# Kernel tuning notes

Hardware: AMD Instinct MI355X
Metric: run time of the kernel (lower is better)

Reference implementation:

```python
import jax, jax.numpy as jnp
import numpy as np

MU, SIGMA = -9.1232, 3.5412
FFT_SIZES = [8, 16, 32, 64]
HOP_SIZES = [2, 4, 8, 16]
EPS_MAG, EPS_SC = 1e-7, 1e-8


def hann_periodic(n):
    # torch.hann_window default (periodic=True)
    return 0.5 * (1.0 - jnp.cos(2.0 * jnp.pi * jnp.arange(n, dtype=jnp.float32) / n))


def stft_mag(xf, n_fft, hop):
    # xf: (rows, T). Matches torch.stft(center=True, pad_mode='reflect', onesided).
    pad = n_fft // 2
    xp = jnp.pad(xf, ((0, 0), (pad, pad)), mode='reflect')
    n_frames = 1 + (xp.shape[-1] - n_fft) // hop
    idx = jnp.arange(n_frames)[:, None] * hop + jnp.arange(n_fft)[None, :]
    frames = xp[:, idx] * hann_periodic(n_fft)  # (rows, n_frames, n_fft)
    spec = jnp.fft.rfft(frames, axis=-1)        # (rows, n_frames, n_fft//2+1)
    return jnp.abs(spec) + EPS_MAG


def setup_inputs() -> dict:
    key = jax.random.key(0)
    k1, k2 = jax.random.split(key)
    x = jax.random.normal(k1, (32, 1, 128, 1024), dtype=jnp.float32)
    y = jax.random.normal(k2, (32, 1, 128, 1024), dtype=jnp.float32)
    return {"x": x, "y": y}


def reference(x, y):
    B, C, F_mel, T = x.shape
    x_flat = jnp.exp(x * SIGMA + MU).reshape(-1, T)  # un-normalize log-mel -> linear
    y_flat = jnp.exp(y * SIGMA + MU).reshape(-1, T)
    loss_sc = jnp.float32(0.0)
    loss_mag = jnp.float32(0.0)
    for n_fft, hop in zip(FFT_SIZES, HOP_SIZES):
        x_mag = stft_mag(x_flat, n_fft, hop)
        y_mag = stft_mag(y_flat, n_fft, hop)
        sc = jnp.linalg.norm((y_mag - x_mag).ravel()) / (
            jnp.linalg.norm(y_mag.ravel()) + EPS_SC)
        mag = jnp.mean(jnp.abs(jnp.log(x_mag) - jnp.log(y_mag)))
        loss_sc = loss_sc + sc
        loss_mag = loss_mag + mag
    n = len(FFT_SIZES)
    return (loss_sc / n, loss_mag / n)
```

## Files before the change

### kernel.cpp

```cpp
#include <hip/hip_runtime.h>
#include <math.h>

static constexpr float kSigma = 3.5412f;
static constexpr float kMu    = -9.1232f;

constexpr double kPId = 3.14159265358979323846264338327950288;

constexpr double tp_sin(double r) {
    const double r2 = r * r;
    double t = r, s = r;
    t *= -r2 / (2.0 * 3.0);   s += t;
    t *= -r2 / (4.0 * 5.0);   s += t;
    t *= -r2 / (6.0 * 7.0);   s += t;
    t *= -r2 / (8.0 * 9.0);   s += t;
    t *= -r2 / (10.0 * 11.0); s += t;
    t *= -r2 / (12.0 * 13.0); s += t;
    return s;
}
constexpr double tp_cos(double r) {
    const double r2 = r * r;
    double t = 1.0, c = 1.0;
    t *= -r2 / (1.0 * 2.0);   c += t;
    t *= -r2 / (3.0 * 4.0);   c += t;
    t *= -r2 / (5.0 * 6.0);   c += t;
    t *= -r2 / (7.0 * 8.0);   c += t;
    t *= -r2 / (9.0 * 10.0);  c += t;
    t *= -r2 / (11.0 * 12.0); c += t;
    return c;
}
constexpr float ctw_c(int k, int n) {
    const int kk = ((k % n) + n) % n;
    const int q = (4 * kk) / n;
    const int num = 4 * kk - q * n;
    const double r = (2.0 * kPId * num) / (4.0 * n);
    const double cr = tp_cos(r), sr = tp_sin(r);
    return (float)(q == 0 ? cr : q == 1 ? -sr : q == 2 ? -cr : sr);
}
constexpr float ctw_ns(int k, int n) {
    const int kk = ((k % n) + n) % n;
    const int q = (4 * kk) / n;
    const int num = 4 * kk - q * n;
    const double r = (2.0 * kPId * num) / (4.0 * n);
    const double cr = tp_cos(r), sr = tp_sin(r);
    const double s = (q == 0 ? sr : q == 1 ? cr : q == 2 ? -sr : -cr);
    return (float)(-s);
}

#define DECLZ \
    float zxr0=0.f,zxi0=0.f,zyr0=0.f,zyi0=0.f,  zxr1=0.f,zxi1=0.f,zyr1=0.f,zyi1=0.f, \
          zxr2=0.f,zxi2=0.f,zyr2=0.f,zyi2=0.f,  zxr3=0.f,zxi3=0.f,zyr3=0.f,zyi3=0.f, \
          zxr4=0.f,zxi4=0.f,zyr4=0.f,zyi4=0.f,  zxr5=0.f,zxi5=0.f,zyr5=0.f,zyi5=0.f, \
          zxr6=0.f,zxi6=0.f,zyr6=0.f,zyi6=0.f,  zxr7=0.f,zxi7=0.f,zyr7=0.f,zyi7=0.f, \
          zxr8=0.f,zxi8=0.f,zyr8=0.f,zyi8=0.f,  zxr9=0.f,zxi9=0.f,zyr9=0.f,zyi9=0.f, \
          zxr10=0.f,zxi10=0.f,zyr10=0.f,zyi10=0.f, zxr11=0.f,zxi11=0.f,zyr11=0.f,zyi11=0.f; \
    (void)zxr0;(void)zxi0;(void)zyr0;(void)zyi0;(void)zxr11;(void)zxi11;(void)zyr11;(void)zyi11;

#define UPDB(n, m) \
    if constexpr ((n) >= 1 && (n) <= NB) { \
        constexpr int   k_ = (BSTART + (n) - 1) * ((m) + TAU * HH); \
        constexpr float c_ = ctw_c(k_, NN); \
        constexpr float s_ = ctw_ns(k_, NN); \
        zxr##n = fmaf(dx, c_, zxr##n);  zxi##n = fmaf(dx, s_, zxi##n); \
        zyr##n = fmaf(dy, c_, zyr##n);  zyi##n = fmaf(dy, s_, zyi##n); \
    }

#define ALLB(m) UPDB(1,m) UPDB(2,m) UPDB(3,m) UPDB(4,m) UPDB(5,m) \
                UPDB(6,m) UPDB(7,m) UPDB(8,m) UPDB(9,m) UPDB(10,m)

#define UPD_M(m) \
    if constexpr ((m) < HH) { \
        const float dx = px[off + TAU*HH + NN + (m)] - px[off + TAU*HH + (m)]; \
        const float dy = py[off + TAU*HH + NN + (m)] - py[off + TAU*HH + (m)]; \
        ALLB(m) \
    }
#define WRM_M(m) \
    if constexpr ((m) < HH) { \
        const float dx = px[TAU*HH + (m)]; \
        const float dy = py[TAU*HH + (m)]; \
        ALLB(m) \
    }

#define FORM(M) M(0) M(1) M(2) M(3) M(4) M(5) M(6) M(7) \
                M(8) M(9) M(10) M(11) M(12) M(13) M(14) M(15)

#define EMTB(nm, nc, np) \
    if constexpr (((nc) - 1) >= EJ0 && ((nc) - 1) < EJ0 + EN) { \
        constexpr int BG = BSTART + (nc) - 1; \
        float wxr, wxi, wyr, wyi; \
        if constexpr (BG == 0) { \
            const float sx_ = (PH==0) ? zxr##np : (PH==1) ? -zxi##np : (PH==2) ? -zxr##np : zxi##np; \
            const float sy_ = (PH==0) ? zyr##np : (PH==1) ? -zyi##np : (PH==2) ? -zyr##np : zyi##np; \
            wxr = 0.5f*zxr##nc - 0.5f*sx_;  wxi = 0.5f*zxi##nc; \
            wyr = 0.5f*zyr##nc - 0.5f*sy_;  wyi = 0.5f*zyi##nc; \
        } else if constexpr (BG == NN/2) { \
            const float sx_ = (PH==0) ? zxr##nm : (PH==1) ? zxi##nm : (PH==2) ? -zxr##nm : -zxi##nm; \
            const float sy_ = (PH==0) ? zyr##nm : (PH==1) ? zyi##nm : (PH==2) ? -zyr##nm : -zyi##nm; \
            wxr = 0.5f*zxr##nc - 0.5f*sx_;  wxi = 0.5f*zxi##nc; \
            wyr = 0.5f*zyr##nc - 0.5f*sy_;  wyi = 0.5f*zyi##nc; \
        } else { \
            const float txr = (PH==0) ? (zxr##nm + zxr##np) : (PH==1) ? (zxi##nm - zxi##np) \
                            : (PH==2) ? (-zxr##nm - zxr##np) : (zxi##np - zxi##nm); \
            const float txi = (PH==0) ? (zxi##nm + zxi##np) : (PH==1) ? (zxr##np - zxr##nm) \
                            : (PH==2) ? (-zxi##nm - zxi##np) : (zxr##nm - zxr##np); \
            const float tyr = (PH==0) ? (zyr##nm + zyr##np) : (PH==1) ? (zyi##nm - zyi##np) \
                            : (PH==2) ? (-zyr##nm - zyr##np) : (zyi##np - zyi##nm); \
            const float tyi = (PH==0) ? (zyi##nm + zyi##np) : (PH==1) ? (zyr##np - zyr##nm) \
                            : (PH==2) ? (-zyi##nm - zyi##np) : (zyr##nm - zyr##np); \
            wxr = fmaf(-0.25f, txr, 0.5f*zxr##nc);  wxi = fmaf(-0.25f, txi, 0.5f*zxi##nc); \
            wyr = fmaf(-0.25f, tyr, 0.5f*zyr##nc);  wyi = fmaf(-0.25f, tyi, 0.5f*zyi##nc); \
        } \
        const float pxm = fmaf(wxr, wxr, wxi*wxi); \
        const float pym = fmaf(wyr, wyr, wyi*wyi); \
        const float sm_ = pxm + pym; \
        const float rt_ = sqrtf(pxm * pym); \
        sd2 += fmaf(-2.0f, rt_, sm_); \
        sy2 += pym; \
        slg = fmaf(0.5f, fabsf(__logf(__fdividef(pxm + 1e-14f, pym + 1e-14f))), slg); \
    }

#define FOREMT(M) M(0,1,2) M(1,2,3) M(2,3,4) M(3,4,5) M(4,5,6) \
                  M(5,6,7) M(6,7,8) M(7,8,9) M(8,9,10) M(9,10,11)

#define SLOT(t) { constexpr int TAU = (t); constexpr int PH = (t); FOREMT(EMTB) FORM(UPD_M) }
#define WARM(t) { constexpr int TAU = (t); FORM(WRM_M) }

template <int NN, int BSTART, int NB, int EJ0, int EN, int OFF>
__device__ __forceinline__ void run_group(const float* __restrict__ px_,
                                          const float* __restrict__ py_,
                                          int seg, float& sd2, float& sy2, float& slg)
{
    constexpr int HH = NN / 4;
    constexpr int FF = 4096 / NN + 1;
    const int t0 = (seg * FF) >> 3;
    const int t1 = ((seg + 1) * FF) >> 3;
    const int L  = t1 - t0;
    const float* __restrict__ px = px_ + OFF + t0 * HH;
    const float* __restrict__ py = py_ + OFF + t0 * HH;

    DECLZ
    WARM(0) WARM(1) WARM(2) WARM(3)

    int off = 0;
    const int nq = L >> 2, rem = L & 3;
#pragma unroll 1
    for (int q = 0; q < nq; ++q) {
        SLOT(0) SLOT(1) SLOT(2) SLOT(3)
        off += 4 * HH;
    }
    if (rem > 0) { SLOT(0) }
    if (rem > 1) { SLOT(1) }
    if (rem > 2) { SLOT(2) }
}

__global__ __launch_bounds__(1024, 4)
void fused_sdft_kernel(const float* __restrict__ xg, const float* __restrict__ yg,
                       float* __restrict__ acc)
{
    constexpr int RS = 1106;
    __shared__ float ldsx[16][RS];
    __shared__ float ldsy[16][RS];
    __shared__ float red[16][3];

    const int tid  = threadIdx.x;
    const int row0 = blockIdx.x << 4;

#pragma unroll 1
    for (int task = tid; task < 8192; task += 1024) {
        const int q = task & 255, rr = (task >> 8) & 15, sig = task >> 12;
        const float* __restrict__ src = sig ? yg : xg;
        const float4 v = reinterpret_cast<const float4*>(src)[((row0 + rr) << 8) + q];
        float* dst = sig ? &ldsy[rr][32 + (q << 2)] : &ldsx[rr][32 + (q << 2)];
        dst[0] = __expf(fmaf(v.x, kSigma, kMu));
        dst[1] = __expf(fmaf(v.y, kSigma, kMu));
        dst[2] = __expf(fmaf(v.z, kSigma, kMu));
        dst[3] = __expf(fmaf(v.w, kSigma, kMu));
    }
#pragma unroll 1
    for (int task = tid; task < 2560; task += 1024) {
        const int p = task % 80, rem_ = task / 80;
        const int rr = rem_ & 15, sig = rem_ >> 4;
        const int j = (p < 32) ? p : (1024 + p);
        float v = 0.f;
        if (j < 1088) {
            const int i = (j < 32) ? (32 - j) : (2078 - j);
            const float* __restrict__ src = sig ? yg : xg;
            v = __expf(fmaf(src[((row0 + rr) << 10) + i], kSigma, kMu));
        }
        (sig ? ldsy[rr] : ldsx[rr])[j] = v;
    }
    __syncthreads();

    const int wid = tid >> 6, lane = tid & 63;
    const int seg = ((wid & 1) << 2) + (lane >> 4);
    const int row = lane & 15;
    const float* lx = &ldsx[row][0];
    const float* ly = &ldsy[row][0];

    float sd2 = 0.f, sy2 = 0.f, slg = 0.f;
    switch (wid >> 1) {
        case 0:  run_group<64,  0,  9, 0, 8,  0>(lx, ly, seg, sd2, sy2, slg); break;
        case 1:  run_group<64,  7, 10, 1, 8,  0>(lx, ly, seg, sd2, sy2, slg); break;
        case 2:  run_group<64, 15, 10, 1, 8,  0>(lx, ly, seg, sd2, sy2, slg); break;
        case 3:  run_group<64, 23, 10, 1, 9,  0>(lx, ly, seg, sd2, sy2, slg); break;
        case 4:  run_group<32,  0,  9, 0, 8, 16>(lx, ly, seg, sd2, sy2, slg); break;
        case 5:  run_group<32,  7, 10, 1, 9, 16>(lx, ly, seg, sd2, sy2, slg); break;
        case 6:  run_group<16,  0,  9, 0, 9, 24>(lx, ly, seg, sd2, sy2, slg); break;
        default: run_group< 8,  0,  5, 0, 5, 28>(lx, ly, seg, sd2, sy2, slg); break;
    }

#pragma unroll
    for (int o = 32; o > 0; o >>= 1) {
        sd2 += __shfl_down(sd2, o);
        sy2 += __shfl_down(sy2, o);
        slg += __shfl_down(slg, o);
    }
    if (lane == 0) { red[wid][0] = sd2; red[wid][1] = sy2; red[wid][2] = slg; }
    __syncthreads();
    if (tid < 16) {
        const int w2 = tid >> 1;
        const int res = (w2 < 4) ? 3 : (w2 < 6) ? 2 : (w2 == 6) ? 1 : 0;
        atomicAdd(&acc[(res * 3 + 0) * 64], red[tid][0]);
        atomicAdd(&acc[(res * 3 + 1) * 64], red[tid][1]);
        atomicAdd(&acc[(res * 3 + 2) * 64], red[tid][2]);
    }
}

__global__ void finalize_kernel(const float* __restrict__ acc, float* __restrict__ out)
{
    if (threadIdx.x == 0 && blockIdx.x == 0) {
        const float nel[4] = {10506240.f, 9474048.f, 8982528.f, 8785920.f};
        float sc = 0.f, mg = 0.f;
#pragma unroll
        for (int r = 0; r < 4; ++r) {
            const float a0 = acc[(r * 3 + 0) * 64];
            const float a1 = acc[(r * 3 + 1) * 64];
            const float a2 = acc[(r * 3 + 2) * 64];
            sc += sqrtf(a0) / (sqrtf(a1) + 1e-8f);
            mg += a2 / nel[r];
        }
        out[0] = sc * 0.25f;
        out[1] = mg * 0.25f;
    }
}

extern "C" void kernel_launch(void* const* d_in, const int* in_sizes, int n_in,
                              void* d_out, int out_size, void* d_ws, size_t ws_size,
                              hipStream_t stream)
{
    const float* x = (const float*)d_in[0];
    const float* y = (const float*)d_in[1];
    float* out = (float*)d_out;
    float* acc = (float*)d_ws;

    hipMemsetAsync(acc, 0, 12 * 64 * sizeof(float), stream);
    fused_sdft_kernel<<<256, 1024, 0, stream>>>(x, y, acc);
    finalize_kernel<<<1, 64, 0, stream>>>(acc, out);
}
```

Baseline: 141.5 us.

## Split x and y signals across lane pairs and double block count

Each thread now runs the sliding DFT for a single signal (x or y) rather than both, and adjacent lanes exchange power values through a shuffle-xor to form the combined metrics. Blocks hold 8 rows instead of 16, and the grid doubles to 512 blocks. Halving the accumulator count per thread is meant to cut register pressure and spread the work over more waves. In exchange, each emitted bin needs a cross-lane shuffle and computes the log term twice, which is corrected by halving in finalize. Scheduling barriers are also inserted every 8 taps to constrain instruction reordering.

```diff
diff --git a/kernel.cpp b/kernel.cpp
--- a/kernel.cpp
+++ b/kernel.cpp
@@ -47,21 +47,17 @@
 }
 
 #define DECLZ \
-    float zxr0=0.f,zxi0=0.f,zyr0=0.f,zyi0=0.f,  zxr1=0.f,zxi1=0.f,zyr1=0.f,zyi1=0.f, \
-          zxr2=0.f,zxi2=0.f,zyr2=0.f,zyi2=0.f,  zxr3=0.f,zxi3=0.f,zyr3=0.f,zyi3=0.f, \
-          zxr4=0.f,zxi4=0.f,zyr4=0.f,zyi4=0.f,  zxr5=0.f,zxi5=0.f,zyr5=0.f,zyi5=0.f, \
-          zxr6=0.f,zxi6=0.f,zyr6=0.f,zyi6=0.f,  zxr7=0.f,zxi7=0.f,zyr7=0.f,zyi7=0.f, \
-          zxr8=0.f,zxi8=0.f,zyr8=0.f,zyi8=0.f,  zxr9=0.f,zxi9=0.f,zyr9=0.f,zyi9=0.f, \
-          zxr10=0.f,zxi10=0.f,zyr10=0.f,zyi10=0.f, zxr11=0.f,zxi11=0.f,zyr11=0.f,zyi11=0.f; \
-    (void)zxr0;(void)zxi0;(void)zyr0;(void)zyi0;(void)zxr11;(void)zxi11;(void)zyr11;(void)zyi11;
+    float zr0=0.f,zi0=0.f, zr1=0.f,zi1=0.f, zr2=0.f,zi2=0.f, zr3=0.f,zi3=0.f, \
+          zr4=0.f,zi4=0.f, zr5=0.f,zi5=0.f, zr6=0.f,zi6=0.f, zr7=0.f,zi7=0.f, \
+          zr8=0.f,zi8=0.f, zr9=0.f,zi9=0.f, zr10=0.f,zi10=0.f, zr11=0.f,zi11=0.f; \
+    (void)zr0;(void)zi0;(void)zr11;(void)zi11;
 
 #define UPDB(n, m) \
     if constexpr ((n) >= 1 && (n) <= NB) { \
         constexpr int   k_ = (BSTART + (n) - 1) * ((m) + TAU * HH); \
         constexpr float c_ = ctw_c(k_, NN); \
         constexpr float s_ = ctw_ns(k_, NN); \
-        zxr##n = fmaf(dx, c_, zxr##n);  zxi##n = fmaf(dx, s_, zxi##n); \
-        zyr##n = fmaf(dy, c_, zyr##n);  zyi##n = fmaf(dy, s_, zyi##n); \
+        zr##n = fmaf(d, c_, zr##n);  zi##n = fmaf(d, s_, zi##n); \
     }
 
 #define ALLB(m) UPDB(1,m) UPDB(2,m) UPDB(3,m) UPDB(4,m) UPDB(5,m) \
@@ -69,15 +65,15 @@
 
 #define UPD_M(m) \
     if constexpr ((m) < HH) { \
-        const float dx = px[off + TAU*HH + NN + (m)] - px[off + TAU*HH + (m)]; \
-        const float dy = py[off + TAU*HH + NN + (m)] - py[off + TAU*HH + (m)]; \
+        const float d = ps[off + TAU*HH + NN + (m)] - ps[off + TAU*HH + (m)]; \
         ALLB(m) \
+        if constexpr (((m) & 7) == 7) __builtin_amdgcn_sched_barrier(0); \
     }
 #define WRM_M(m) \
     if constexpr ((m) < HH) { \
-        const float dx = px[TAU*HH + (m)]; \
-        const float dy = py[TAU*HH + (m)]; \
+        const float d = ps[TAU*HH + (m)]; \
         ALLB(m) \
+        if constexpr (((m) & 7) == 7) __builtin_amdgcn_sched_barrier(0); \
     }
 
 #define FORM(M) M(0) M(1) M(2) M(3) M(4) M(5) M(6) M(7) \
@@ -86,36 +82,27 @@
 #define EMTB(nm, nc, np) \
     if constexpr (((nc) - 1) >= EJ0 && ((nc) - 1) < EJ0 + EN) { \
         constexpr int BG = BSTART + (nc) - 1; \
-        float wxr, wxi, wyr, wyi; \
+        float wr, wi; \
         if constexpr (BG == 0) { \
-            const float sx_ = (PH==0) ? zxr##np : (PH==1) ? -zxi##np : (PH==2) ? -zxr##np : zxi##np; \
-            const float sy_ = (PH==0) ? zyr##np : (PH==1) ? -zyi##np : (PH==2) ? -zyr##np : zyi##np; \
-            wxr = 0.5f*zxr##nc - 0.5f*sx_;  wxi = 0.5f*zxi##nc; \
-            wyr = 0.5f*zyr##nc - 0.5f*sy_;  wyi = 0.5f*zyi##nc; \
+            const float s_ = (PH==0) ? zr##np : (PH==1) ? -zi##np : (PH==2) ? -zr##np : zi##np; \
+            wr = 0.5f*zr##nc - 0.5f*s_;  wi = 0.5f*zi##nc; \
         } else if constexpr (BG == NN/2) { \
-            const float sx_ = (PH==0) ? zxr##nm : (PH==1) ? zxi##nm : (PH==2) ? -zxr##nm : -zxi##nm; \
-            const float sy_ = (PH==0) ? zyr##nm : (PH==1) ? zyi##nm : (PH==2) ? -zyr##nm : -zyi##nm; \
-            wxr = 0.5f*zxr##nc - 0.5f*sx_;  wxi = 0.5f*zxi##nc; \
-            wyr = 0.5f*zyr##nc - 0.5f*sy_;  wyi = 0.5f*zyi##nc; \
+            const float s_ = (PH==0) ? zr##nm : (PH==1) ? zi##nm : (PH==2) ? -zr##nm : -zi##nm; \
+            wr = 0.5f*zr##nc - 0.5f*s_;  wi = 0.5f*zi##nc; \
         } else { \
-            const float txr = (PH==0) ? (zxr##nm + zxr##np) : (PH==1) ? (zxi##nm - zxi##np) \
-                            : (PH==2) ? (-zxr##nm - zxr##np) : (zxi##np - zxi##nm); \
-            const float txi = (PH==0) ? (zxi##nm + zxi##np) : (PH==1) ? (zxr##np - zxr##nm) \
-                            : (PH==2) ? (-zxi##nm - zxi##np) : (zxr##nm - zxr##np); \
-            const float tyr = (PH==0) ? (zyr##nm + zyr##np) : (PH==1) ? (zyi##nm - zyi##np) \
-                            : (PH==2) ? (-zyr##nm - zyr##np) : (zyi##np - zyi##nm); \
-            const float tyi = (PH==0) ? (zyi##nm + zyi##np) : (PH==1) ? (zyr##np - zyr##nm) \
-                            : (PH==2) ? (-zyi##nm - zyi##np) : (zyr##nm - zyr##np); \
-            wxr = fmaf(-0.25f, txr, 0.5f*zxr##nc);  wxi = fmaf(-0.25f, txi, 0.5f*zxi##nc); \
-            wyr = fmaf(-0.25f, tyr, 0.5f*zyr##nc);  wyi = fmaf(-0.25f, tyi, 0.5f*zyi##nc); \
+            const float tr = (PH==0) ? (zr##nm + zr##np) : (PH==1) ? (zi##nm - zi##np) \
+                           : (PH==2) ? (-zr##nm - zr##np) : (zi##np - zi##nm); \
+            const float ti = (PH==0) ? (zi##nm + zi##np) : (PH==1) ? (zr##np - zr##nm) \
+                           : (PH==2) ? (-zi##nm - zi##np) : (zr##nm - zr##np); \
+            wr = fmaf(-0.25f, tr, 0.5f*zr##nc);  wi = fmaf(-0.25f, ti, 0.5f*zi##nc); \
         } \
-        const float pxm = fmaf(wxr, wxr, wxi*wxi); \
-        const float pym = fmaf(wyr, wyr, wyi*wyi); \
-        const float sm_ = pxm + pym; \
-        const float rt_ = sqrtf(pxm * pym); \
+        const float pm = fmaf(wr, wr, wi*wi); \
+        const float po = __shfl_xor(pm, 1); \
+        const float sm_ = pm + po; \
+        const float rt_ = sqrtf(pm * po); \
         sd2 += fmaf(-2.0f, rt_, sm_); \
-        sy2 += pym; \
-        slg = fmaf(0.5f, fabsf(__logf(__fdividef(pxm + 1e-14f, pym + 1e-14f))), slg); \
+        sy2 += sig ? pm : po; \
+        slg = fmaf(0.5f, fabsf(__logf(__fdividef(pm + 1e-14f, po + 1e-14f))), slg); \
     }
 
 #define FOREMT(M) M(0,1,2) M(1,2,3) M(2,3,4) M(3,4,5) M(4,5,6) \
@@ -125,17 +112,16 @@
 #define WARM(t) { constexpr int TAU = (t); FORM(WRM_M) }
 
 template <int NN, int BSTART, int NB, int EJ0, int EN, int OFF>
-__device__ __forceinline__ void run_group(const float* __restrict__ px_,
-                                          const float* __restrict__ py_,
-                                          int seg, float& sd2, float& sy2, float& slg)
+__device__ __forceinline__ void run_group(const float* __restrict__ ps_,
+                                          int seg, int sig,
+                                          float& sd2, float& sy2, float& slg)
 {
     constexpr int HH = NN / 4;
     constexpr int FF = 4096 / NN + 1;
     const int t0 = (seg * FF) >> 3;
     const int t1 = ((seg + 1) * FF) >> 3;
     const int L  = t1 - t0;
-    const float* __restrict__ px = px_ + OFF + t0 * HH;
-    const float* __restrict__ py = py_ + OFF + t0 * HH;
+    const float* __restrict__ ps = ps_ + OFF + t0 * HH;
 
     DECLZ
     WARM(0) WARM(1) WARM(2) WARM(3)
@@ -157,55 +143,56 @@
                        float* __restrict__ acc)
 {
     constexpr int RS = 1106;
-    __shared__ float ldsx[16][RS];
-    __shared__ float ldsy[16][RS];
+    __shared__ float ldsx[8][RS];
+    __shared__ float ldsy[8][RS];
     __shared__ float red[16][3];
 
     const int tid  = threadIdx.x;
-    const int row0 = blockIdx.x << 4;
+    const int row0 = blockIdx.x << 3;
 
 #pragma unroll 1
-    for (int task = tid; task < 8192; task += 1024) {
-        const int q = task & 255, rr = (task >> 8) & 15, sig = task >> 12;
-        const float* __restrict__ src = sig ? yg : xg;
+    for (int task = tid; task < 4096; task += 1024) {
+        const int q = task & 255, rr = (task >> 8) & 7, sg = task >> 11;
+        const float* __restrict__ src = sg ? yg : xg;
         const float4 v = reinterpret_cast<const float4*>(src)[((row0 + rr) << 8) + q];
-        float* dst = sig ? &ldsy[rr][32 + (q << 2)] : &ldsx[rr][32 + (q << 2)];
+        float* dst = (sg ? &ldsy[rr][0] : &ldsx[rr][0]) + 32 + (q << 2);
         dst[0] = __expf(fmaf(v.x, kSigma, kMu));
         dst[1] = __expf(fmaf(v.y, kSigma, kMu));
         dst[2] = __expf(fmaf(v.z, kSigma, kMu));
         dst[3] = __expf(fmaf(v.w, kSigma, kMu));
     }
 #pragma unroll 1
-    for (int task = tid; task < 2560; task += 1024) {
+    for (int task = tid; task < 1280; task += 1024) {
         const int p = task % 80, rem_ = task / 80;
-        const int rr = rem_ & 15, sig = rem_ >> 4;
+        const int rr = rem_ & 7, sg = rem_ >> 3;
         const int j = (p < 32) ? p : (1024 + p);
         float v = 0.f;
         if (j < 1088) {
             const int i = (j < 32) ? (32 - j) : (2078 - j);
-            const float* __restrict__ src = sig ? yg : xg;
+            const float* __restrict__ src = sg ? yg : xg;
             v = __expf(fmaf(src[((row0 + rr) << 10) + i], kSigma, kMu));
         }
-        (sig ? ldsy[rr] : ldsx[rr])[j] = v;
+        (sg ? ldsy[rr] : ldsx[rr])[j] = v;
     }
     __syncthreads();
 
-    const int wid = tid >> 6, lane = tid & 63;
-    const int seg = ((wid & 1) << 2) + (lane >> 4);
-    const int row = lane & 15;
-    const float* lx = &ldsx[row][0];
-    const float* ly = &ldsy[row][0];
+    const int wid  = tid >> 6, lane = tid & 63;
+    const int idx  = ((wid & 1) << 6) | lane;
+    const int seg  = idx >> 4;
+    const int row  = (idx >> 1) & 7;
+    const int sig  = idx & 1;
+    const float* ps = sig ? &ldsy[row][0] : &ldsx[row][0];
 
     float sd2 = 0.f, sy2 = 0.f, slg = 0.f;
     switch (wid >> 1) {
-        case 0:  run_group<64,  0,  9, 0, 8,  0>(lx, ly, seg, sd2, sy2, slg); break;
-        case 1:  run_group<64,  7, 10, 1, 8,  0>(lx, ly, seg, sd2, sy2, slg); break;
-        case 2:  run_group<64, 15, 10, 1, 8,  0>(lx, ly, seg, sd2, sy2, slg); break;
-        case 3:  run_group<64, 23, 10, 1, 9,  0>(lx, ly, seg, sd2, sy2, slg); break;
-        case 4:  run_group<32,  0,  9, 0, 8, 16>(lx, ly, seg, sd2, sy2, slg); break;
-        case 5:  run_group<32,  7, 10, 1, 9, 16>(lx, ly, seg, sd2, sy2, slg); break;
-        case 6:  run_group<16,  0,  9, 0, 9, 24>(lx, ly, seg, sd2, sy2, slg); break;
-        default: run_group< 8,  0,  5, 0, 5, 28>(lx, ly, seg, sd2, sy2, slg); break;
+        case 0:  run_group<64,  0,  9, 0, 8,  0>(ps, seg, sig, sd2, sy2, slg); break;
+        case 1:  run_group<64,  7, 10, 1, 8,  0>(ps, seg, sig, sd2, sy2, slg); break;
+        case 2:  run_group<64, 15, 10, 1, 8,  0>(ps, seg, sig, sd2, sy2, slg); break;
+        case 3:  run_group<64, 23, 10, 1, 9,  0>(ps, seg, sig, sd2, sy2, slg); break;
+        case 4:  run_group<32,  0,  9, 0, 8, 16>(ps, seg, sig, sd2, sy2, slg); break;
+        case 5:  run_group<32,  7, 10, 1, 9, 16>(ps, seg, sig, sd2, sy2, slg); break;
+        case 6:  run_group<16,  0,  9, 0, 9, 24>(ps, seg, sig, sd2, sy2, slg); break;
+        default: run_group< 8,  0,  5, 0, 5, 28>(ps, seg, sig, sd2, sy2, slg); break;
     }
 
 #pragma unroll
@@ -236,7 +223,7 @@
             const float a1 = acc[(r * 3 + 1) * 64];
             const float a2 = acc[(r * 3 + 2) * 64];
             sc += sqrtf(a0) / (sqrtf(a1) + 1e-8f);
-            mg += a2 / nel[r];
+            mg += a2 * 0.5f / nel[r];
         }
         out[0] = sc * 0.25f;
         out[1] = mg * 0.25f;
@@ -253,6 +240,6 @@
     float* acc = (float*)d_ws;
 
     hipMemsetAsync(acc, 0, 12 * 64 * sizeof(float), stream);
-    fused_sdft_kernel<<<256, 1024, 0, stream>>>(x, y, acc);
+    fused_sdft_kernel<<<512, 1024, 0, stream>>>(x, y, acc);
     finalize_kernel<<<1, 64, 0, stream>>>(acc, out);
 }
```

After: 216.4 us. 1.53x slower.
